# Kernel tuning notes

Measured on AMD Instinct MI355X. Metric: run time of the kernel, lower is better.

## Reference

```python
import jax, jax.numpy as jnp
import numpy as np

H = 12          # number_of_heads
D = 768         # embedding_dim
DH = D // H     # head dim = 64
P = 14          # sqrt(num_patches) for image_size=224, patch=16
B, S = 64, 197  # batch, seq (196 patches + CLS)


def setup_inputs() -> dict:
    key = jax.random.key(0)
    ks = jax.random.split(key, 7)
    scale = 1.0 / np.sqrt(D)
    return {
        "q": jax.random.normal(ks[0], (B, S, D), jnp.float32),
        "k": jax.random.normal(ks[1], (B, S, D), jnp.float32),
        "v": jax.random.normal(ks[2], (B, S, D), jnp.float32),
        # nn.Linear weights, stored as [out, in]; applied as x @ W.T
        "Wq": jax.random.normal(ks[3], (D, D), jnp.float32) * scale,
        "Wk": jax.random.normal(ks[4], (D, D), jnp.float32) * scale,
        "Wv": jax.random.normal(ks[5], (D, D), jnp.float32) * scale,
        "Wo": jax.random.normal(ks[6], (D, D), jnp.float32) * scale,
    }


def reference(q, k, v, Wq, Wk, Wv, Wo):
    # Linear projections (bias=False): x @ W.T
    def proj(x, W):
        # [B,S,D] -> [B,H,S,DH]
        y = jnp.einsum('bsd,ed->bse', x, W)
        return y.reshape(B, S, H, DH).transpose(0, 2, 1, 3)

    qh, kh, vh = proj(q, Wq), proj(k, Wk), proj(v, Wv)

    # raw scores [B,H,S,S]
    scores = jnp.einsum('bhqd,bhkd->bhqk', qh, kh) / jnp.sqrt(jnp.asarray(DH, qh.dtype))
    attn = jax.nn.softmax(scores, axis=-1)

    # CLS (row 0) attention to the 196 patches -> [B,H,P,P]
    cls_to_patch_map = attn[:, :, 0, 1:].reshape(B, H, P, P)

    # dropout in eval mode (identity; deterministic reference)
    x = jnp.einsum('bhqk,bhkd->bhqd', attn, vh)          # [B,H,S,DH]
    x = x.transpose(0, 2, 1, 3).reshape(B, S, D)          # [B,S,D]
    output = jnp.einsum('bsd,ed->bse', x, Wo)
    return output, cls_to_patch_map
```

## Files before the change

### kernel.cpp

```cpp
#include <hip/hip_runtime.h>
#include <hip/hip_bf16.h>
#include <stdint.h>

#define DI __device__ __forceinline__

constexpr int Bn = 64;
constexpr int S  = 197;
constexpr int Dm = 768;
constexpr int H  = 12;
constexpr int DH = 64;
constexpr int M  = Bn * S;
constexpr int SP = 224;
constexpr int MD = M * Dm;
constexpr int WN = Dm * Dm;

typedef __attribute__((ext_vector_type(8))) short bf8;
typedef __attribute__((ext_vector_type(4))) float f4;

DI ushort f2bf(float f) {
  union { __hip_bfloat16 b; ushort u; } cv;
  cv.b = __float2bfloat16(f);
  return cv.u;
}

DI void gload_lds16(const void* g, const void* lds) {
  __builtin_amdgcn_global_load_lds(
      (__attribute__((address_space(1))) void*)(uintptr_t)g,
      (__attribute__((address_space(3))) void*)(uint32_t)(uintptr_t)lds,
      16, 0, 0);
}

DI bf8 ld16(const ushort* p) { return *(const bf8*)p; }

__global__ __launch_bounds__(256) void convert_all(
    const float4* __restrict__ q,  const float4* __restrict__ k,
    const float4* __restrict__ v,  const float4* __restrict__ wq,
    const float4* __restrict__ wk, const float4* __restrict__ wv,
    const float4* __restrict__ wo,
    ushort4* __restrict__ qb, ushort4* __restrict__ kb,
    ushort4* __restrict__ vb, ushort4* __restrict__ wb) {
  constexpr int NT = MD / 4;
  constexpr int NW = WN / 4;
  int i = blockIdx.x * 256 + threadIdx.x;
  const float4* src; ushort4* dst; int off;
  if (i < NT)            { src = q; dst = qb; off = i; }
  else if (i < 2 * NT)   { src = k; dst = kb; off = i - NT; }
  else if (i < 3 * NT)   { src = v; dst = vb; off = i - 2 * NT; }
  else {
    int j = i - 3 * NT;
    int wsel = j / NW; off = j - wsel * NW;
    src = wsel == 0 ? wq : wsel == 1 ? wk : wsel == 2 ? wv : wo;
    dst = wb + (size_t)wsel * NW;
  }
  float4 f = src[off];
  ushort4 u;
  u.x = f2bf(f.x); u.y = f2bf(f.y); u.z = f2bf(f.z); u.w = f2bf(f.w);
  dst[off] = u;
}

template <int MODE>
__global__ __launch_bounds__(256) void gemm_bt(
    const ushort* __restrict__ Abase, const ushort* __restrict__ Wbase,
    ushort* __restrict__ OQK, ushort* __restrict__ OV, float* __restrict__ OF) {
  __shared__ __align__(16) ushort As[128 * 32];
  __shared__ __align__(16) ushort Ws[128 * 32];
  const int tid  = threadIdx.x;
  const int lane = tid & 63;
  const int w    = tid >> 6;
  const int wr   = w >> 1, wc = w & 1;
  const int rsel = lane & 15, g = lane >> 4;
  const int m0 = blockIdx.x * 128, n0 = blockIdx.y * 128;
  const int z  = blockIdx.z;
  const ushort* A = Abase + (MODE == 0 ? (size_t)z * MD : 0);
  const ushort* W = Wbase + (MODE == 0 ? (size_t)z * WN : 0);

  const f4 fz = {0.f, 0.f, 0.f, 0.f};
  f4 acc[4][4];
#pragma unroll
  for (int i = 0; i < 4; i++)
#pragma unroll
    for (int j = 0; j < 4; j++) acc[i][j] = fz;

  const int row0 = tid >> 2,        ko0 = (tid & 3) * 8;
  const int row1 = 64 + (tid >> 2), ko1 = ko0;
  int ar0 = m0 + row0; if (ar0 >= M) ar0 = M - 1;
  int ar1 = m0 + row1; if (ar1 >= M) ar1 = M - 1;
  const int wbase = (tid & ~63) * 8;

  for (int k0 = 0; k0 < Dm; k0 += 32) {
    gload_lds16(A + (size_t)ar0 * Dm + k0 + ko0, As + wbase);
    gload_lds16(A + (size_t)ar1 * Dm + k0 + ko1, As + 2048 + wbase);
    gload_lds16(W + (size_t)(n0 + row0) * Dm + k0 + ko0, Ws + wbase);
    gload_lds16(W + (size_t)(n0 + row1) * Dm + k0 + ko1, Ws + 2048 + wbase);
    __syncthreads();
    bf8 af[4], wf[4];
#pragma unroll
    for (int i = 0; i < 4; i++)
      af[i] = ld16(&As[(wr * 64 + i * 16 + rsel) * 32 + g * 8]);
#pragma unroll
    for (int j = 0; j < 4; j++)
      wf[j] = ld16(&Ws[(wc * 64 + j * 16 + rsel) * 32 + g * 8]);
#pragma unroll
    for (int i = 0; i < 4; i++)
#pragma unroll
      for (int j = 0; j < 4; j++)
        acc[i][j] = __builtin_amdgcn_mfma_f32_16x16x32_bf16(af[i], wf[j], acc[i][j], 0, 0, 0);
    __syncthreads();
  }

#pragma unroll
  for (int i = 0; i < 4; i++) {
    const int mb = m0 + wr * 64 + i * 16 + g * 4;
#pragma unroll
    for (int j = 0; j < 4; j++) {
      const int n = n0 + wc * 64 + j * 16 + rsel;
#pragma unroll
      for (int rg = 0; rg < 4; rg++) {
        const int m = mb + rg;
        if (m < M) {
          const float val = acc[i][j][rg];
          if (MODE == 1) {
            OF[(size_t)m * Dm + n] = val;
          } else {
            const int b = m / S, s = m - b * S;
            const int hh = n >> 6, dh = n & 63;
            const ushort bv = f2bf(val);
            if (z < 2)
              OQK[(size_t)z * MD + (((size_t)b * H + hh) * S + s) * DH + dh] = bv;
            else
              OV[(((size_t)b * H + hh) * DH + dh) * SP + s] = bv;
          }
        }
      }
    }
  }
}

__global__ __launch_bounds__(256) void attn_fwd(
    const ushort* __restrict__ Qh, const ushort* __restrict__ Kh,
    const ushort* __restrict__ Vt, ushort* __restrict__ xh,
    float* __restrict__ outcls) {
  __shared__ __align__(16) ushort Pl[4][16][232];
  const int bh = blockIdx.x;
  const int b = bh / H, h = bh - b * H;
  const int tid = threadIdx.x, lane = tid & 63, w = tid >> 6;
  const int rsel = lane & 15, g = lane >> 4;
  const f4 fz = {0.f, 0.f, 0.f, 0.f};

#pragma unroll
  for (int t = 0; t < 6; t++) {
    int idx = t * 64 + lane;
    Pl[w][idx / 24][208 + idx % 24] = 0;
  }

  const ushort* Qs = Qh + (size_t)bh * S * DH;
  const ushort* Ks = Kh + (size_t)bh * S * DH;
  const ushort* Vs = Vt + (size_t)bh * DH * SP;

  for (int qt = w; qt < 13; qt += 4) {
    const int q0 = qt * 16;
    int qrow = q0 + rsel; if (qrow > S - 1) qrow = S - 1;
    const bf8 aq0 = ld16(Qs + qrow * DH + g * 8);
    const bf8 aq1 = ld16(Qs + qrow * DH + 32 + g * 8);

    f4 sc[13];
#pragma unroll
    for (int kt = 0; kt < 13; kt++) {
      int key = kt * 16 + rsel; if (key > S - 1) key = S - 1;
      const bf8 bk0 = ld16(Ks + key * DH + g * 8);
      const bf8 bk1 = ld16(Ks + key * DH + 32 + g * 8);
      f4 a = fz;
      a = __builtin_amdgcn_mfma_f32_16x16x32_bf16(aq0, bk0, a, 0, 0, 0);
      a = __builtin_amdgcn_mfma_f32_16x16x32_bf16(aq1, bk1, a, 0, 0, 0);
      sc[kt] = a * 0.125f;
    }

    float mx[4] = {-1e30f, -1e30f, -1e30f, -1e30f};
#pragma unroll
    for (int kt = 0; kt < 13; kt++) {
      const bool vmask = (kt * 16 + rsel) < S;
#pragma unroll
      for (int r = 0; r < 4; r++)
        if (vmask) mx[r] = fmaxf(mx[r], sc[kt][r]);
    }
#pragma unroll
    for (int d = 1; d < 16; d <<= 1)
#pragma unroll
      for (int r = 0; r < 4; r++) mx[r] = fmaxf(mx[r], __shfl_xor(mx[r], d));
    float sm[4] = {0.f, 0.f, 0.f, 0.f};
#pragma unroll
    for (int kt = 0; kt < 13; kt++) {
      const bool vmask = (kt * 16 + rsel) < S;
#pragma unroll
      for (int r = 0; r < 4; r++) {
        const float p = vmask ? exp2f((sc[kt][r] - mx[r]) * 1.44269504f) : 0.f;
        sc[kt][r] = p;
        sm[r] += p;
      }
    }
#pragma unroll
    for (int d = 1; d < 16; d <<= 1)
#pragma unroll
      for (int r = 0; r < 4; r++) sm[r] += __shfl_xor(sm[r], d);

    if (qt == 0 && g == 0) {
      const float inv0 = 1.f / sm[0];
#pragma unroll
      for (int kt = 0; kt < 13; kt++) {
        const int key = kt * 16 + rsel;
        if (key >= 1 && key < S)
          outcls[(size_t)bh * 196 + key - 1] = sc[kt][0] * inv0;
      }
    }

#pragma unroll
    for (int kt = 0; kt < 13; kt++)
#pragma unroll
      for (int r = 0; r < 4; r++)
        Pl[w][g * 4 + r][kt * 16 + rsel] = f2bf(sc[kt][r]);

    bf8 pa[7];
#pragma unroll
    for (int kc = 0; kc < 7; kc++)
      pa[kc] = ld16(&Pl[w][rsel][kc * 32 + g * 8]);
    float inv[4];
#pragma unroll
    for (int r = 0; r < 4; r++) inv[r] = 1.f / sm[r];
#pragma unroll
    for (int nt = 0; nt < 4; nt++) {
      f4 x = fz;
#pragma unroll
      for (int kc = 0; kc < 7; kc++) {
        const bf8 bv = ld16(Vs + (nt * 16 + rsel) * SP + kc * 32 + g * 8);
        x = __builtin_amdgcn_mfma_f32_16x16x32_bf16(pa[kc], bv, x, 0, 0, 0);
      }
#pragma unroll
      for (int r = 0; r < 4; r++) {
        const int s_ = q0 + g * 4 + r;
        if (s_ < S)
          xh[((size_t)b * S + s_) * Dm + h * DH + nt * 16 + rsel] = f2bf(x[r] * inv[r]);
      }
    }
  }
}

extern "C" void kernel_launch(void* const* d_in, const int* in_sizes, int n_in,
                              void* d_out, int out_size, void* d_ws, size_t ws_size,
                              hipStream_t stream) {
  (void)in_sizes; (void)n_in; (void)out_size; (void)ws_size;
  const float* q  = (const float*)d_in[0];
  const float* k  = (const float*)d_in[1];
  const float* v  = (const float*)d_in[2];
  const float* wq = (const float*)d_in[3];
  const float* wk = (const float*)d_in[4];
  const float* wv = (const float*)d_in[5];
  const float* wo = (const float*)d_in[6];

  uint8_t* ws = (uint8_t*)d_ws;
  ushort* qb = (ushort*)ws;
  ushort* kb = qb + (size_t)MD;
  ushort* vb = kb + (size_t)MD;
  ushort* wb = vb + (size_t)MD;
  ushort* Qh = wb + 4 * (size_t)WN;
  ushort* Kh = Qh + (size_t)MD;
  ushort* Vt = Kh + (size_t)MD;
  ushort* xh = qb;

  float* out    = (float*)d_out;
  float* outcls = out + (size_t)MD;

  hipMemsetAsync(Vt, 0, (size_t)Bn * H * DH * SP * sizeof(ushort), stream);

  constexpr int CONV_BLOCKS = (3 * (MD / 4) + 4 * (WN / 4)) / 256;
  convert_all<<<dim3(CONV_BLOCKS), 256, 0, stream>>>(
      (const float4*)q, (const float4*)k, (const float4*)v,
      (const float4*)wq, (const float4*)wk, (const float4*)wv, (const float4*)wo,
      (ushort4*)qb, (ushort4*)kb, (ushort4*)vb, (ushort4*)wb);

  gemm_bt<0><<<dim3(99, 6, 3), 256, 0, stream>>>(qb, wb, Qh, Vt, nullptr);

  attn_fwd<<<dim3(Bn * H), 256, 0, stream>>>(Qh, Kh, Vt, xh, outcls);

  gemm_bt<1><<<dim3(99, 6, 1), 256, 0, stream>>>(xh, wb + 3 * (size_t)WN, nullptr, nullptr, out);
}
```

Baseline: 360.9 us.

## Rewrite projection GEMMs as 256x256 double-buffered tiles with swizzled LDS

Replaces the 128x128 single-buffered bf16 GEMM with a 512-thread 256x256-tile kernel. It double-buffers 64-wide K slabs in LDS, prefetching the next slab between MFMA groups and gating with explicit vmcnt waits and barriers, and XOR-swizzles the LDS layout to avoid bank conflicts. It also raises wave priority around MFMA bursts. This aims to hide global load latency and improve data reuse per block, at the cost of fewer blocks (150 per GEMM z-slice), more wasted rows in the last M tile, and higher register and LDS pressure.

```diff
diff --git a/kernel.cpp b/kernel.cpp
--- a/kernel.cpp
+++ b/kernel.cpp
@@ -13,6 +13,7 @@
 constexpr int SP = 224;
 constexpr int MD = M * Dm;
 constexpr int WN = Dm * Dm;
+constexpr int NKT = Dm / 64;
 
 typedef __attribute__((ext_vector_type(8))) short bf8;
 typedef __attribute__((ext_vector_type(4))) float f4;
@@ -31,6 +32,9 @@
 }
 
 DI bf8 ld16(const ushort* p) { return *(const bf8*)p; }
+
+#define GATE4 asm volatile("s_waitcnt vmcnt(4) lgkmcnt(0)\ns_barrier" ::: "memory")
+#define GATE0 asm volatile("s_waitcnt vmcnt(0) lgkmcnt(0)\ns_barrier" ::: "memory")
 
 __global__ __launch_bounds__(256) void convert_all(
     const float4* __restrict__ q,  const float4* __restrict__ k,
@@ -58,59 +62,108 @@
   dst[off] = u;
 }
 
+
+DI void stage_half(const ushort* __restrict__ src, int rowmax, int row0,
+                   int kcol0, ushort* lds_half, int w, int lane) {
+#pragma unroll
+  for (int l = 0; l < 2; ++l) {
+    const int cc = w * 2 + l;
+    const int rl = cc * 16 + (lane >> 2);
+    int rg = row0 + rl; if (rg > rowmax) rg = rowmax;
+    const int k8 = (lane & 3) ^ ((rl >> 1) & 3);
+    gload_lds16(src + (size_t)rg * Dm + kcol0 + k8 * 8, lds_half + cc * 512);
+  }
+}
+
+DI bf8 ldfrag(const ushort* half_, int row, int g) {
+  return ld16(half_ + row * 32 + ((g ^ ((row >> 1) & 3)) << 3));
+}
+
 template <int MODE>
-__global__ __launch_bounds__(256) void gemm_bt(
+__global__ __launch_bounds__(512, 2) void gemm8(
     const ushort* __restrict__ Abase, const ushort* __restrict__ Wbase,
     ushort* __restrict__ OQK, ushort* __restrict__ OV, float* __restrict__ OF) {
-  __shared__ __align__(16) ushort As[128 * 32];
-  __shared__ __align__(16) ushort Ws[128 * 32];
-  const int tid  = threadIdx.x;
-  const int lane = tid & 63;
-  const int w    = tid >> 6;
-  const int wr   = w >> 1, wc = w & 1;
+  __shared__ __align__(16) ushort As[2][2][256 * 32];
+  __shared__ __align__(16) ushort Bs[2][2][256 * 32];
+  const int tid = threadIdx.x, lane = tid & 63, w = tid >> 6;
+  const int wr = w >> 2, wc = w & 3;
   const int rsel = lane & 15, g = lane >> 4;
-  const int m0 = blockIdx.x * 128, n0 = blockIdx.y * 128;
-  const int z  = blockIdx.z;
+  const int n0 = blockIdx.x * 256, m0 = blockIdx.y * 256, z = blockIdx.z;
   const ushort* A = Abase + (MODE == 0 ? (size_t)z * MD : 0);
   const ushort* W = Wbase + (MODE == 0 ? (size_t)z * WN : 0);
 
   const f4 fz = {0.f, 0.f, 0.f, 0.f};
-  f4 acc[4][4];
-#pragma unroll
-  for (int i = 0; i < 4; i++)
+  f4 acc[8][4];
+#pragma unroll
+  for (int i = 0; i < 8; i++)
 #pragma unroll
     for (int j = 0; j < 4; j++) acc[i][j] = fz;
 
-  const int row0 = tid >> 2,        ko0 = (tid & 3) * 8;
-  const int row1 = 64 + (tid >> 2), ko1 = ko0;
-  int ar0 = m0 + row0; if (ar0 >= M) ar0 = M - 1;
-  int ar1 = m0 + row1; if (ar1 >= M) ar1 = M - 1;
-  const int wbase = (tid & ~63) * 8;
-
-  for (int k0 = 0; k0 < Dm; k0 += 32) {
-    gload_lds16(A + (size_t)ar0 * Dm + k0 + ko0, As + wbase);
-    gload_lds16(A + (size_t)ar1 * Dm + k0 + ko1, As + 2048 + wbase);
-    gload_lds16(W + (size_t)(n0 + row0) * Dm + k0 + ko0, Ws + wbase);
-    gload_lds16(W + (size_t)(n0 + row1) * Dm + k0 + ko1, Ws + 2048 + wbase);
-    __syncthreads();
-    bf8 af[4], wf[4];
-#pragma unroll
-    for (int i = 0; i < 4; i++)
-      af[i] = ld16(&As[(wr * 64 + i * 16 + rsel) * 32 + g * 8]);
-#pragma unroll
-    for (int j = 0; j < 4; j++)
-      wf[j] = ld16(&Ws[(wc * 64 + j * 16 + rsel) * 32 + g * 8]);
-#pragma unroll
-    for (int i = 0; i < 4; i++)
-#pragma unroll
-      for (int j = 0; j < 4; j++)
-        acc[i][j] = __builtin_amdgcn_mfma_f32_16x16x32_bf16(af[i], wf[j], acc[i][j], 0, 0, 0);
-    __syncthreads();
-  }
-
-#pragma unroll
-  for (int i = 0; i < 4; i++) {
-    const int mb = m0 + wr * 64 + i * 16 + g * 4;
+  stage_half(A, M - 1, m0, 0,  &As[0][0][0], w, lane);
+  stage_half(W, 767,   n0, 0,  &Bs[0][0][0], w, lane);
+  stage_half(A, M - 1, m0, 32, &As[0][1][0], w, lane);
+  stage_half(W, 767,   n0, 32, &Bs[0][1][0], w, lane);
+
+  for (int kt = 0; kt < NKT; ++kt) {
+    const int cur = kt & 1, nxt = cur ^ 1;
+    const bool pf = kt < NKT - 1;
+    const int kc = (kt + 1) * 64;
+    bf8 a[4], b[4];
+
+    GATE4;
+#pragma unroll
+    for (int i = 0; i < 4; ++i) a[i] = ldfrag(&As[cur][0][0], wr * 128 + i * 16 + rsel, g);
+#pragma unroll
+    for (int j = 0; j < 4; ++j) b[j] = ldfrag(&Bs[cur][0][0], wc * 64 + j * 16 + rsel, g);
+    if (pf) stage_half(A, M - 1, m0, kc, &As[nxt][0][0], w, lane);
+    __builtin_amdgcn_s_setprio(1);
+#pragma unroll
+    for (int i = 0; i < 4; ++i)
+#pragma unroll
+      for (int j = 0; j < 4; ++j)
+        acc[i][j] = __builtin_amdgcn_mfma_f32_16x16x32_bf16(a[i], b[j], acc[i][j], 0, 0, 0);
+    __builtin_amdgcn_s_setprio(0);
+
+#pragma unroll
+    for (int i = 0; i < 4; ++i) a[i] = ldfrag(&As[cur][0][0], wr * 128 + (4 + i) * 16 + rsel, g);
+    if (pf) stage_half(W, 767, n0, kc, &Bs[nxt][0][0], w, lane);
+    __builtin_amdgcn_s_setprio(1);
+#pragma unroll
+    for (int i = 0; i < 4; ++i)
+#pragma unroll
+      for (int j = 0; j < 4; ++j)
+        acc[4 + i][j] = __builtin_amdgcn_mfma_f32_16x16x32_bf16(a[i], b[j], acc[4 + i][j], 0, 0, 0);
+    __builtin_amdgcn_s_setprio(0);
+
+    if (kt == NKT - 1) { GATE0; } else { GATE4; }
+#pragma unroll
+    for (int i = 0; i < 4; ++i) a[i] = ldfrag(&As[cur][1][0], wr * 128 + i * 16 + rsel, g);
+#pragma unroll
+    for (int j = 0; j < 4; ++j) b[j] = ldfrag(&Bs[cur][1][0], wc * 64 + j * 16 + rsel, g);
+    if (pf) stage_half(A, M - 1, m0, kc + 32, &As[nxt][1][0], w, lane);
+    __builtin_amdgcn_s_setprio(1);
+#pragma unroll
+    for (int i = 0; i < 4; ++i)
+#pragma unroll
+      for (int j = 0; j < 4; ++j)
+        acc[i][j] = __builtin_amdgcn_mfma_f32_16x16x32_bf16(a[i], b[j], acc[i][j], 0, 0, 0);
+    __builtin_amdgcn_s_setprio(0);
+
+#pragma unroll
+    for (int i = 0; i < 4; ++i) a[i] = ldfrag(&As[cur][1][0], wr * 128 + (4 + i) * 16 + rsel, g);
+    if (pf) stage_half(W, 767, n0, kc + 32, &Bs[nxt][1][0], w, lane);
+    __builtin_amdgcn_s_setprio(1);
+#pragma unroll
+    for (int i = 0; i < 4; ++i)
+#pragma unroll
+      for (int j = 0; j < 4; ++j)
+        acc[4 + i][j] = __builtin_amdgcn_mfma_f32_16x16x32_bf16(a[i], b[j], acc[4 + i][j], 0, 0, 0);
+    __builtin_amdgcn_s_setprio(0);
+  }
+
+#pragma unroll
+  for (int i = 0; i < 8; i++) {
+    const int mb = m0 + wr * 128 + i * 16 + g * 4;
 #pragma unroll
     for (int j = 0; j < 4; j++) {
       const int n = n0 + wc * 64 + j * 16 + rsel;
@@ -277,9 +330,9 @@
       (const float4*)wq, (const float4*)wk, (const float4*)wv, (const float4*)wo,
       (ushort4*)qb, (ushort4*)kb, (ushort4*)vb, (ushort4*)wb);
 
-  gemm_bt<0><<<dim3(99, 6, 3), 256, 0, stream>>>(qb, wb, Qh, Vt, nullptr);
+  gemm8<0><<<dim3(3, 50, 3), 512, 0, stream>>>(qb, wb, Qh, Vt, nullptr);
 
   attn_fwd<<<dim3(Bn * H), 256, 0, stream>>>(Qh, Kh, Vt, xh, outcls);
 
-  gemm_bt<1><<<dim3(99, 6, 1), 256, 0, stream>>>(xh, wb + 3 * (size_t)WN, nullptr, nullptr, out);
-}
+  gemm8<1><<<dim3(3, 50, 1), 512, 0, stream>>>(xh, wb + 3 * (size_t)WN, nullptr, nullptr, out);
+}
```

Measured after the change: 331.8 us. 8.0% less time.

## Double-buffer GEMM LDS tiles with swizzle and XCD-aware block remap

Applied to the files above, without the earlier changes.

Replaces the single-buffered projection GEMM with a double-buffered version that prefetches the next K tile into LDS while MFMAs consume the current one, using one barrier per K step. It XOR-swizzles the LDS layout to reduce bank conflicts on fragment loads and remaps the 1D block index so neighbouring tiles land on the same XCD for L2 reuse. It also sets MFMA priority and an occupancy hint of 3 blocks. The cost is doubled LDS use, and the hand-placed waitcnt/barrier ordering is fragile.

```diff
diff --git a/kernel.cpp b/kernel.cpp
--- a/kernel.cpp
+++ b/kernel.cpp
@@ -58,21 +58,66 @@
   dst[off] = u;
 }
 
+
+DI void stage128(const ushort* __restrict__ src, int rowmax, int row0,
+                 int kcol0, ushort* lds, int w, int lane) {
+#pragma unroll
+  for (int l = 0; l < 2; ++l) {
+    const int cid = w * 2 + l;
+    const int c = cid * 64 + lane;
+    const int rl = c >> 2;
+    int rg = row0 + rl; if (rg > rowmax) rg = rowmax;
+    const int k8 = (c & 3) ^ ((rl >> 1) & 3);
+    gload_lds16(src + (size_t)rg * Dm + kcol0 + k8 * 8, lds + cid * 512);
+  }
+}
+
+DI bf8 ldfrag(const ushort* buf, int row, int g) {
+  return ld16(buf + row * 32 + ((g ^ ((row >> 1) & 3)) << 3));
+}
+
+#define KSTEP(KT, CUR, NXT)                                               \
+  {                                                                       \
+    if ((KT) < 23) {                                                      \
+      stage128(A, M - 1, m0, ((KT) + 1) * 32, As[NXT], w, lane);          \
+      stage128(W, 767, n0, ((KT) + 1) * 32, Bs[NXT], w, lane);            \
+    }                                                                     \
+    bf8 a[4], b[4];                                                       \
+    _Pragma("unroll") for (int i = 0; i < 4; ++i)                         \
+        a[i] = ldfrag(As[CUR], wr * 64 + i * 16 + rsel, g);               \
+    _Pragma("unroll") for (int j = 0; j < 4; ++j)                         \
+        b[j] = ldfrag(Bs[CUR], wc * 64 + j * 16 + rsel, g);               \
+    __builtin_amdgcn_s_setprio(1);                                        \
+    _Pragma("unroll") for (int i = 0; i < 4; ++i)                         \
+      _Pragma("unroll") for (int j = 0; j < 4; ++j)                       \
+        acc[i][j] = __builtin_amdgcn_mfma_f32_16x16x32_bf16(              \
+            a[i], b[j], acc[i][j], 0, 0, 0);                              \
+    __builtin_amdgcn_s_setprio(0);                                        \
+    asm volatile("s_waitcnt vmcnt(0) lgkmcnt(0)" ::: "memory");           \
+    __builtin_amdgcn_s_barrier();                                         \
+  }
+
 template <int MODE>
-__global__ __launch_bounds__(256) void gemm_bt(
-    const ushort* __restrict__ Abase, const ushort* __restrict__ Wbase,
+__global__ __launch_bounds__(256, 3) void gemmL(
+    const ushort* __restrict__ Ab, const ushort* __restrict__ Wb,
     ushort* __restrict__ OQK, ushort* __restrict__ OV, float* __restrict__ OF) {
-  __shared__ __align__(16) ushort As[128 * 32];
-  __shared__ __align__(16) ushort Ws[128 * 32];
-  const int tid  = threadIdx.x;
-  const int lane = tid & 63;
-  const int w    = tid >> 6;
-  const int wr   = w >> 1, wc = w & 1;
+  __shared__ __align__(16) ushort As[2][128 * 32];
+  __shared__ __align__(16) ushort Bs[2][128 * 32];
+  constexpr int NT  = 6;
+  constexpr int NWG = 594;
+  const int tid = threadIdx.x, lane = tid & 63, w = tid >> 6;
+  const int wr = w >> 1, wc = w & 1;
   const int rsel = lane & 15, g = lane >> 4;
-  const int m0 = blockIdx.x * 128, n0 = blockIdx.y * 128;
-  const int z  = blockIdx.z;
-  const ushort* A = Abase + (MODE == 0 ? (size_t)z * MD : 0);
-  const ushort* W = Wbase + (MODE == 0 ? (size_t)z * WN : 0);
+
+  constexpr int qq = NWG / 8, rr = NWG % 8;
+  const int bid = blockIdx.x;
+  const int xcd = bid & 7, pos = bid >> 3;
+  const int wg = (xcd < rr ? xcd * (qq + 1) : rr * (qq + 1) + (xcd - rr) * qq) + pos;
+  const int nt = wg % NT, mt = wg / NT;
+  const int n0 = nt * 128, m0 = mt * 128;
+  const int z = blockIdx.y;
+  const ushort* A = Ab + (size_t)z * MD;
+  const ushort* W = Wb + (size_t)z * WN;
 
   const f4 fz = {0.f, 0.f, 0.f, 0.f};
   f4 acc[4][4];
@@ -81,31 +126,16 @@
 #pragma unroll
     for (int j = 0; j < 4; j++) acc[i][j] = fz;
 
-  const int row0 = tid >> 2,        ko0 = (tid & 3) * 8;
-  const int row1 = 64 + (tid >> 2), ko1 = ko0;
-  int ar0 = m0 + row0; if (ar0 >= M) ar0 = M - 1;
-  int ar1 = m0 + row1; if (ar1 >= M) ar1 = M - 1;
-  const int wbase = (tid & ~63) * 8;
-
-  for (int k0 = 0; k0 < Dm; k0 += 32) {
-    gload_lds16(A + (size_t)ar0 * Dm + k0 + ko0, As + wbase);
-    gload_lds16(A + (size_t)ar1 * Dm + k0 + ko1, As + 2048 + wbase);
-    gload_lds16(W + (size_t)(n0 + row0) * Dm + k0 + ko0, Ws + wbase);
-    gload_lds16(W + (size_t)(n0 + row1) * Dm + k0 + ko1, Ws + 2048 + wbase);
-    __syncthreads();
-    bf8 af[4], wf[4];
-#pragma unroll
-    for (int i = 0; i < 4; i++)
-      af[i] = ld16(&As[(wr * 64 + i * 16 + rsel) * 32 + g * 8]);
-#pragma unroll
-    for (int j = 0; j < 4; j++)
-      wf[j] = ld16(&Ws[(wc * 64 + j * 16 + rsel) * 32 + g * 8]);
-#pragma unroll
-    for (int i = 0; i < 4; i++)
-#pragma unroll
-      for (int j = 0; j < 4; j++)
-        acc[i][j] = __builtin_amdgcn_mfma_f32_16x16x32_bf16(af[i], wf[j], acc[i][j], 0, 0, 0);
-    __syncthreads();
+  stage128(A, M - 1, m0, 0, As[0], w, lane);
+  stage128(W, 767, n0, 0, Bs[0], w, lane);
+  asm volatile("s_waitcnt vmcnt(0)" ::: "memory");
+  __builtin_amdgcn_s_barrier();
+
+#pragma unroll 1
+  for (int kt2 = 0; kt2 < 12; ++kt2) {
+    const int kt = kt2 * 2;
+    KSTEP(kt, 0, 1);
+    KSTEP(kt + 1, 1, 0);
   }
 
 #pragma unroll
@@ -277,9 +307,9 @@
       (const float4*)wq, (const float4*)wk, (const float4*)wv, (const float4*)wo,
       (ushort4*)qb, (ushort4*)kb, (ushort4*)vb, (ushort4*)wb);
 
-  gemm_bt<0><<<dim3(99, 6, 3), 256, 0, stream>>>(qb, wb, Qh, Vt, nullptr);
+  gemmL<0><<<dim3(594, 3), 256, 0, stream>>>(qb, wb, Qh, Vt, nullptr);
 
   attn_fwd<<<dim3(Bn * H), 256, 0, stream>>>(Qh, Kh, Vt, xh, outcls);
 
-  gemm_bt<1><<<dim3(99, 6, 1), 256, 0, stream>>>(xh, wb + 3 * (size_t)WN, nullptr, nullptr, out);
-}
+  gemmL<1><<<dim3(594, 1), 256, 0, stream>>>(xh, wb + 3 * (size_t)WN, nullptr, nullptr, out);
+}
```

Result: faster. 318.5 us (-11.7%).
